# Performance work log

Hardware: AMD Instinct MI355X
Metric: run time of the kernel (lower is better)

Reference implementation:

```python
import jax, jax.numpy as jnp
import numpy as np

LUT_DIM = 33
CTX_DIM = 128


def _identity_lut(dim):
    coords = jnp.linspace(0.0, 1.0, dim)
    r, g, b = jnp.meshgrid(coords, coords, coords, indexing='ij')
    return jnp.stack([r, g, b], axis=-1)  # [dim, dim, dim, 3], axes (r,g,b)


def setup_inputs() -> dict:
    key = jax.random.key(0)
    ks = jax.random.split(key, 8)
    B, H, W = 4, 512, 512
    image = jax.random.normal(ks[0], (B, 3, H, W), dtype=jnp.float32)
    spatial_context = jax.random.normal(ks[1], (B, CTX_DIM, H, W), dtype=jnp.float32)
    s = 0.05
    params = {
        'base_lut': _identity_lut(LUT_DIM),
        'W1': jax.random.normal(ks[2], (128, CTX_DIM), dtype=jnp.float32) * s,
        'b1': jnp.zeros((128,), dtype=jnp.float32),
        'W2': jax.random.normal(ks[3], (64, 128), dtype=jnp.float32) * s,
        'b2': jnp.zeros((64,), dtype=jnp.float32),
        'W3': jax.random.normal(ks[4], (3, 64), dtype=jnp.float32) * s,
        'b3': jnp.zeros((3,), dtype=jnp.float32),
        'offset_scale': jnp.float32(0.1),
    }
    return {'image': image, 'spatial_context': spatial_context, **params}


def _conv1x1(x, W, b):
    # x: [B,Cin,H,W], W: [Cout,Cin]
    return jnp.einsum('bchw,oc->bohw', x, W) + b[None, :, None, None]


def _trilinear_lut(lut_flat, gx, gy, gz, dim):
    # lut_flat: [3, dim^3] (flattened over z,y,x = r,g,b axes)
    # gx,gy,gz: [B,H,W] float coords in [0, dim-1]; border padding via clamp
    fmax = jnp.float32(dim - 1)
    gx = jnp.clip(gx, 0.0, fmax)
    gy = jnp.clip(gy, 0.0, fmax)
    gz = jnp.clip(gz, 0.0, fmax)
    x0 = jnp.floor(gx).astype(jnp.int32)
    y0 = jnp.floor(gy).astype(jnp.int32)
    z0 = jnp.floor(gz).astype(jnp.int32)
    x1 = jnp.minimum(x0 + 1, dim - 1)
    y1 = jnp.minimum(y0 + 1, dim - 1)
    z1 = jnp.minimum(z0 + 1, dim - 1)
    fx = gx - x0.astype(gx.dtype)
    fy = gy - y0.astype(gy.dtype)
    fz = gz - z0.astype(gz.dtype)

    def gather(zi, yi, xi):
        idx = (zi * dim + yi) * dim + xi  # [B,H,W]
        return lut_flat[:, idx]  # [3,B,H,W]

    c000 = gather(z0, y0, x0); c001 = gather(z0, y0, x1)
    c010 = gather(z0, y1, x0); c011 = gather(z0, y1, x1)
    c100 = gather(z1, y0, x0); c101 = gather(z1, y0, x1)
    c110 = gather(z1, y1, x0); c111 = gather(z1, y1, x1)

    fx = fx[None]; fy = fy[None]; fz = fz[None]
    c00 = c000 * (1 - fx) + c001 * fx
    c01 = c010 * (1 - fx) + c011 * fx
    c10 = c100 * (1 - fx) + c101 * fx
    c11 = c110 * (1 - fx) + c111 * fx
    c0 = c00 * (1 - fy) + c01 * fy
    c1 = c10 * (1 - fy) + c11 * fy
    out = c0 * (1 - fz) + c1 * fz  # [3,B,H,W]
    return jnp.transpose(out, (1, 0, 2, 3))  # [B,3,H,W]


def reference(image, spatial_context, base_lut, W1, b1, W2, b2, W3, b3, offset_scale):
    dim = base_lut.shape[0]
    gelu = lambda v: jax.nn.gelu(v, approximate=False)
    h = gelu(_conv1x1(spatial_context, W1, b1))
    h = gelu(_conv1x1(h, W2, b2))
    offset = jnp.tanh(_conv1x1(h, W3, b3)) * offset_scale  # [B,3,H,W]

    img01 = jnp.clip((image + 1.0) * 0.5, 0.0, 1.0)
    # grid_sample convention: grid channel0 (R)->x->last LUT axis (b),
    # channel1 (G)->y->g axis, channel2 (B)->z->r axis; align_corners=True.
    scale = jnp.float32(dim - 1)
    gx = img01[:, 0] * scale  # R -> b axis
    gy = img01[:, 1] * scale  # G -> g axis
    gz = img01[:, 2] * scale  # B -> r axis
    # base_lut [r,g,b,3] -> channels-first [3, r(=z), g(=y), b(=x)] -> flatten
    lut_flat = jnp.transpose(base_lut, (3, 0, 1, 2)).reshape(3, dim * dim * dim)
    sampled = _trilinear_lut(lut_flat, gx, gy, gz, dim)  # [B,3,H,W]
    return sampled * 2.0 - 1.0 + offset
```

## Files before the change

kernel.cpp:

```cpp
#include <hip/hip_runtime.h>
#include <stdint.h>

#define HW 262144
#define LDIM 33

typedef __bf16 bf16x8 __attribute__((ext_vector_type(8)));
typedef __bf16 bf16x2 __attribute__((ext_vector_type(2)));
typedef float  f32x4  __attribute__((ext_vector_type(4)));

union BF8 { bf16x8 v; unsigned u[4]; };

__device__ __forceinline__ unsigned pk2(float a, float b) {
  bf16x2 p; p[0] = (__bf16)a; p[1] = (__bf16)b;
  return __builtin_bit_cast(unsigned, p);
}
__device__ __forceinline__ float exp2_hw(float x) {
  return __builtin_amdgcn_exp2f(x);
}
__device__ __forceinline__ float tanh_fast(float x) {
  float t = exp2_hw(x * 2.8853900818f);
  return 1.0f - __fdividef(2.0f, t + 1.0f);
}
__device__ __forceinline__ float gelu_t(float x) {
  float x2 = x * x;
  float p2 = x * fmaf(0.1029425216f, x2, 2.3021667f);
  float r  = __fdividef(1.0f, exp2_hw(p2) + 1.0f);
  return fmaf(-x, r, x);
}

__global__ __launch_bounds__(256, 2) void local3dlut_kernel(
    const float* __restrict__ img,  const float* __restrict__ ctx,
    const float* __restrict__ lut,  const float* __restrict__ W1,
    const float* __restrict__ b1,   const float* __restrict__ W2,
    const float* __restrict__ b2,   const float* __restrict__ W3,
    const float* __restrict__ b3,   const float* __restrict__ oscp,
    float* __restrict__ out)
{
  __shared__ uint4 smem4[3584];
  char* sm = (char*)smem4;
  const int t    = threadIdx.x;
  const int lane = t & 63;
  const int wv   = t >> 6;
  const int n    = lane & 15;
  const int q    = lane >> 4;

  #pragma unroll
  for (int rep = 0; rep < 16; ++rep) {
    int f4 = t + 256 * rep;
    float4 v = ((const float4*)W1)[f4];
    int fi = f4 << 2;
    int o = fi >> 7, k = fi & 127;
    char* dst = sm + o * 256 + (((k >> 3) ^ (o & 15)) << 4) + ((k & 7) << 1);
    *(uint2*)dst = make_uint2(pk2(v.x, v.y), pk2(v.z, v.w));
  }
  #pragma unroll
  for (int rep = 0; rep < 8; ++rep) {
    int f4 = t + 256 * rep;
    float4 v = ((const float4*)W2)[f4];
    int fi = f4 << 2;
    int o = fi >> 7, k = fi & 127;
    char* dst = sm + 32768 + o * 256 + (((k >> 3) ^ (o & 15)) << 4) + ((k & 7) << 1);
    *(uint2*)dst = make_uint2(pk2(v.x, v.y), pk2(v.z, v.w));
  }
  __syncthreads();

  float b1l[8][4];
  #pragma unroll
  for (int i = 0; i < 8; ++i)
    #pragma unroll
    for (int r = 0; r < 4; ++r) b1l[i][r] = b1[i * 16 + (q << 2) + r];
  float b2l[4][4];
  #pragma unroll
  for (int i = 0; i < 4; ++i)
    #pragma unroll
    for (int r = 0; r < 4; ++r) b2l[i][r] = b2[i * 16 + (q << 2) + r];
  BF8 w3a[2];
  #pragma unroll
  for (int ks3 = 0; ks3 < 2; ++ks3) {
    #pragma unroll
    for (int m = 0; m < 4; ++m) {
      float e0 = 0.f, e1 = 0.f;
      if (n < 3) {
        e0 = W3[n * 64 + ks3 * 32 + q * 8 + 2 * m];
        e1 = W3[n * 64 + ks3 * 32 + q * 8 + 2 * m + 1];
      }
      w3a[ks3].u[m] = pk2(e0, e1);
    }
  }
  const float b3a0 = b3[0], b3a1 = b3[1], b3a2 = b3[2];
  const float osc  = oscp[0];

  const int p0   = blockIdx.x * 512;
  const int bi   = p0 >> 18;
  const int sblk = p0 & (HW - 1);
  const float* ctxB = ctx + (size_t)bi * ((size_t)128 * HW);
  const float* imgB = img + (size_t)bi * ((size_t)3 * HW);
  float*       outB = out + (size_t)bi * ((size_t)3 * HW);
  char* hb = sm + 49152 + wv * 2048;
  char* hrow = hb + n * 128;
  const int nsw = n & 7;
  const int woff = (q & 1) << 3;

  #pragma unroll 1
  for (int it = 0; it < 8; ++it) {
    const int sw = sblk + it * 64 + wv * 16;

    const int spf = sw + n;
    const float rr = imgB[spf];
    const float gg = imgB[HW + spf];
    const float bb = imgB[2 * HW + spf];

    BF8 a1[4];
    {
      const int sA = sw + n;
      #pragma unroll
      for (int ks = 0; ks < 4; ++ks) {
        const float* cb = ctxB + (size_t)(ks * 32 + q * 8) * HW + sA;
        float v0 = cb[0];
        float v1 = cb[(size_t)1 * HW];
        float v2 = cb[(size_t)2 * HW];
        float v3 = cb[(size_t)3 * HW];
        float v4 = cb[(size_t)4 * HW];
        float v5 = cb[(size_t)5 * HW];
        float v6 = cb[(size_t)6 * HW];
        float v7 = cb[(size_t)7 * HW];
        a1[ks].u[0] = pk2(v0, v1);
        a1[ks].u[1] = pk2(v2, v3);
        a1[ks].u[2] = pk2(v4, v5);
        a1[ks].u[3] = pk2(v6, v7);
      }
    }

    float fx, fy, fz;
    float c000, c001, c010, c011, c100, c101, c110, c111;
    {
      float gx = fminf(fmaxf(fmaf(rr, 16.f, 16.f), 0.f), 32.f);
      float gy = fminf(fmaxf(fmaf(gg, 16.f, 16.f), 0.f), 32.f);
      float gz = fminf(fmaxf(fmaf(bb, 16.f, 16.f), 0.f), 32.f);
      int x0 = (int)gx, y0 = (int)gy, z0 = (int)gz;
      fx = gx - (float)x0; fy = gy - (float)y0; fz = gz - (float)z0;
      int x1 = min(x0 + 1, 32), y1 = min(y0 + 1, 32), z1 = min(z0 + 1, 32);
      int zy00 = (z0 * LDIM + y0) * LDIM, zy01 = (z0 * LDIM + y1) * LDIM;
      int zy10 = (z1 * LDIM + y0) * LDIM, zy11 = (z1 * LDIM + y1) * LDIM;
      const int chq = (q < 3) ? q : 2;
      const float* L = lut;
      c000 = L[(zy00 + x0) * 3 + chq]; c001 = L[(zy00 + x1) * 3 + chq];
      c010 = L[(zy01 + x0) * 3 + chq]; c011 = L[(zy01 + x1) * 3 + chq];
      c100 = L[(zy10 + x0) * 3 + chq]; c101 = L[(zy10 + x1) * 3 + chq];
      c110 = L[(zy11 + x0) * 3 + chq]; c111 = L[(zy11 + x1) * 3 + chq];
    }

    f32x4 acc2[4];
    #pragma unroll
    for (int j = 0; j < 4; ++j) { f32x4 z = {0.f,0.f,0.f,0.f}; acc2[j] = z; }

    #pragma unroll
    for (int half = 0; half < 2; ++half) {
      f32x4 acc1[4];
      #pragma unroll
      for (int j = 0; j < 4; ++j) { f32x4 z = {0.f,0.f,0.f,0.f}; acc1[j] = z; }

      #pragma unroll
      for (int ks = 0; ks < 4; ++ks) {
        #pragma unroll
        for (int nt4 = 0; nt4 < 4; ++nt4) {
          int row = (half * 4 + nt4) * 16 + n;
          bf16x8 bw = *(const bf16x8*)(sm + row * 256 + ((((ks << 2) + q) ^ n) << 4));
          acc1[nt4] = __builtin_amdgcn_mfma_f32_16x16x32_bf16(bw, a1[ks].v, acc1[nt4], 0, 0, 0);
        }
      }
      #pragma unroll
      for (int nt4 = 0; nt4 < 4; ++nt4) {
        float g0 = gelu_t(acc1[nt4][0] + b1l[half * 4 + nt4][0]);
        float g1 = gelu_t(acc1[nt4][1] + b1l[half * 4 + nt4][1]);
        float g2 = gelu_t(acc1[nt4][2] + b1l[half * 4 + nt4][2]);
        float g3 = gelu_t(acc1[nt4][3] + b1l[half * 4 + nt4][3]);
        int kg = (nt4 << 1) + (q >> 1);
        char* dst = hrow + ((kg ^ nsw) << 4) + woff;
        *(uint2*)dst = make_uint2(pk2(g0, g1), pk2(g2, g3));
      }
      #pragma unroll
      for (int ks2 = 0; ks2 < 2; ++ks2) {
        bf16x8 a2 = *(const bf16x8*)(hrow + ((((ks2 << 2) + q) ^ nsw) << 4));
        #pragma unroll
        for (int nt2 = 0; nt2 < 4; ++nt2) {
          int row = nt2 * 16 + n;
          int kg2 = half * 8 + (ks2 << 2) + q;
          bf16x8 bw = *(const bf16x8*)(sm + 32768 + row * 256 + ((kg2 ^ n) << 4));
          acc2[nt2] = __builtin_amdgcn_mfma_f32_16x16x32_bf16(bw, a2, acc2[nt2], 0, 0, 0);
        }
      }
    }

    #pragma unroll
    for (int nt2 = 0; nt2 < 4; ++nt2) {
      float g0 = gelu_t(acc2[nt2][0] + b2l[nt2][0]);
      float g1 = gelu_t(acc2[nt2][1] + b2l[nt2][1]);
      float g2 = gelu_t(acc2[nt2][2] + b2l[nt2][2]);
      float g3 = gelu_t(acc2[nt2][3] + b2l[nt2][3]);
      int kg = (nt2 << 1) + (q >> 1);
      char* dst = hrow + ((kg ^ nsw) << 4) + woff;
      *(uint2*)dst = make_uint2(pk2(g0, g1), pk2(g2, g3));
    }

    f32x4 acc3 = {0.f, 0.f, 0.f, 0.f};
    #pragma unroll
    for (int ks3 = 0; ks3 < 2; ++ks3) {
      bf16x8 hf = *(const bf16x8*)(hrow + ((((ks3 << 2) + q) ^ nsw) << 4));
      acc3 = __builtin_amdgcn_mfma_f32_16x16x32_bf16(w3a[ks3].v, hf, acc3, 0, 0, 0);
    }
    const int ba = n << 2;
    float d0 = __int_as_float(__builtin_amdgcn_ds_bpermute(ba, __float_as_int(acc3[0])));
    float d1 = __int_as_float(__builtin_amdgcn_ds_bpermute(ba, __float_as_int(acc3[1])));
    float d2 = __int_as_float(__builtin_amdgcn_ds_bpermute(ba, __float_as_int(acc3[2])));

    if (q < 3) {
      float sel  = (q == 0) ? d0   : ((q == 1) ? d1   : d2);
      float bsel = (q == 0) ? b3a0 : ((q == 1) ? b3a1 : b3a2);
      float ov = tanh_fast(sel + bsel) * osc;

      float c00 = c000 + fx * (c001 - c000);
      float c01 = c010 + fx * (c011 - c010);
      float c10 = c100 + fx * (c101 - c100);
      float c11 = c110 + fx * (c111 - c110);
      float ca  = c00 + fy * (c01 - c00);
      float cb2 = c10 + fy * (c11 - c10);
      float so  = ca + fz * (cb2 - ca);
      outB[q * HW + sw + n] = so * 2.f - 1.f + ov;
    }
  }
}

extern "C" void kernel_launch(void* const* d_in, const int* in_sizes, int n_in,
                              void* d_out, int out_size, void* d_ws, size_t ws_size,
                              hipStream_t stream) {
  const float* img = (const float*)d_in[0];
  const float* ctx = (const float*)d_in[1];
  const float* lut = (const float*)d_in[2];
  const float* W1  = (const float*)d_in[3];
  const float* b1  = (const float*)d_in[4];
  const float* W2  = (const float*)d_in[5];
  const float* b2  = (const float*)d_in[6];
  const float* W3  = (const float*)d_in[7];
  const float* b3  = (const float*)d_in[8];
  const float* osc = (const float*)d_in[9];
  float* out = (float*)d_out;
  local3dlut_kernel<<<dim3(2048), dim3(256), 0, stream>>>(
      img, ctx, lut, W1, b1, W2, b2, W3, b3, osc, out);
}
```

Before: 777.3 us.

## Split fused MLP kernel into GEMM1 kernel and tail kernel via workspace

Splits the single fused kernel in two. The first computes conv1+GELU and writes a bf16 hidden tensor (256 B per pixel, about 268 MB total) to workspace, and the second reads it back for conv2, conv3, the LUT interpolation and the output. The aim is to cut per-kernel LDS and register pressure so occupancy rises. The cost is a large extra global-memory round trip. The fused kernel remains as a fallback when the workspace is too small.

```diff
diff --git a/kernel.cpp b/kernel.cpp
--- a/kernel.cpp
+++ b/kernel.cpp
@@ -28,15 +28,11 @@
   return fmaf(-x, r, x);
 }
 
-__global__ __launch_bounds__(256, 2) void local3dlut_kernel(
-    const float* __restrict__ img,  const float* __restrict__ ctx,
-    const float* __restrict__ lut,  const float* __restrict__ W1,
-    const float* __restrict__ b1,   const float* __restrict__ W2,
-    const float* __restrict__ b2,   const float* __restrict__ W3,
-    const float* __restrict__ b3,   const float* __restrict__ oscp,
-    float* __restrict__ out)
+__global__ __launch_bounds__(256, 2) void gemm1_h1_kernel(
+    const float* __restrict__ ctx, const float* __restrict__ W1,
+    const float* __restrict__ b1,  char* __restrict__ h1)
 {
-  __shared__ uint4 smem4[3584];
+  __shared__ uint4 smem4[2048];
   char* sm = (char*)smem4;
   const int t    = threadIdx.x;
   const int lane = t & 63;
@@ -53,15 +49,6 @@
     char* dst = sm + o * 256 + (((k >> 3) ^ (o & 15)) << 4) + ((k & 7) << 1);
     *(uint2*)dst = make_uint2(pk2(v.x, v.y), pk2(v.z, v.w));
   }
-  #pragma unroll
-  for (int rep = 0; rep < 8; ++rep) {
-    int f4 = t + 256 * rep;
-    float4 v = ((const float4*)W2)[f4];
-    int fi = f4 << 2;
-    int o = fi >> 7, k = fi & 127;
-    char* dst = sm + 32768 + o * 256 + (((k >> 3) ^ (o & 15)) << 4) + ((k & 7) << 1);
-    *(uint2*)dst = make_uint2(pk2(v.x, v.y), pk2(v.z, v.w));
-  }
   __syncthreads();
 
   float b1l[8][4];
@@ -69,46 +56,16 @@
   for (int i = 0; i < 8; ++i)
     #pragma unroll
     for (int r = 0; r < 4; ++r) b1l[i][r] = b1[i * 16 + (q << 2) + r];
-  float b2l[4][4];
-  #pragma unroll
-  for (int i = 0; i < 4; ++i)
-    #pragma unroll
-    for (int r = 0; r < 4; ++r) b2l[i][r] = b2[i * 16 + (q << 2) + r];
-  BF8 w3a[2];
-  #pragma unroll
-  for (int ks3 = 0; ks3 < 2; ++ks3) {
-    #pragma unroll
-    for (int m = 0; m < 4; ++m) {
-      float e0 = 0.f, e1 = 0.f;
-      if (n < 3) {
-        e0 = W3[n * 64 + ks3 * 32 + q * 8 + 2 * m];
-        e1 = W3[n * 64 + ks3 * 32 + q * 8 + 2 * m + 1];
-      }
-      w3a[ks3].u[m] = pk2(e0, e1);
-    }
-  }
-  const float b3a0 = b3[0], b3a1 = b3[1], b3a2 = b3[2];
-  const float osc  = oscp[0];
 
   const int p0   = blockIdx.x * 512;
   const int bi   = p0 >> 18;
   const int sblk = p0 & (HW - 1);
   const float* ctxB = ctx + (size_t)bi * ((size_t)128 * HW);
-  const float* imgB = img + (size_t)bi * ((size_t)3 * HW);
-  float*       outB = out + (size_t)bi * ((size_t)3 * HW);
-  char* hb = sm + 49152 + wv * 2048;
-  char* hrow = hb + n * 128;
-  const int nsw = n & 7;
-  const int woff = (q & 1) << 3;
 
   #pragma unroll 1
   for (int it = 0; it < 8; ++it) {
     const int sw = sblk + it * 64 + wv * 16;
-
-    const int spf = sw + n;
-    const float rr = imgB[spf];
-    const float gg = imgB[HW + spf];
-    const float bb = imgB[2 * HW + spf];
+    const int gp = p0 + it * 64 + wv * 16 + n;
 
     BF8 a1[4];
     {
@@ -131,6 +88,105 @@
       }
     }
 
+    f32x4 acc[8];
+    #pragma unroll
+    for (int j = 0; j < 8; ++j) { f32x4 z = {0.f,0.f,0.f,0.f}; acc[j] = z; }
+    #pragma unroll
+    for (int ks = 0; ks < 4; ++ks) {
+      #pragma unroll
+      for (int nt = 0; nt < 8; ++nt) {
+        int row = nt * 16 + n;
+        bf16x8 bw = *(const bf16x8*)(sm + row * 256 + ((((ks << 2) + q) ^ n) << 4));
+        acc[nt] = __builtin_amdgcn_mfma_f32_16x16x32_bf16(bw, a1[ks].v, acc[nt], 0, 0, 0);
+      }
+    }
+
+    char* hrow = h1 + (size_t)gp * 256;
+    #pragma unroll
+    for (int nt = 0; nt < 8; ++nt) {
+      float g0 = gelu_t(acc[nt][0] + b1l[nt][0]);
+      float g1 = gelu_t(acc[nt][1] + b1l[nt][1]);
+      float g2 = gelu_t(acc[nt][2] + b1l[nt][2]);
+      float g3 = gelu_t(acc[nt][3] + b1l[nt][3]);
+      *(uint2*)(hrow + nt * 32 + (q << 3)) = make_uint2(pk2(g0, g1), pk2(g2, g3));
+    }
+  }
+}
+
+__global__ __launch_bounds__(256, 2) void mlp_tail_kernel(
+    const float* __restrict__ img, const float* __restrict__ lut,
+    const char* __restrict__ h1,   const float* __restrict__ W2,
+    const float* __restrict__ b2,  const float* __restrict__ W3,
+    const float* __restrict__ b3,  const float* __restrict__ oscp,
+    float* __restrict__ out)
+{
+  __shared__ uint4 smem4[1536];
+  char* sm = (char*)smem4;
+  const int t    = threadIdx.x;
+  const int lane = t & 63;
+  const int wv   = t >> 6;
+  const int n    = lane & 15;
+  const int q    = lane >> 4;
+
+  #pragma unroll
+  for (int rep = 0; rep < 8; ++rep) {
+    int f4 = t + 256 * rep;
+    float4 v = ((const float4*)W2)[f4];
+    int fi = f4 << 2;
+    int o = fi >> 7, k = fi & 127;
+    char* dst = sm + o * 256 + (((k >> 3) ^ (o & 15)) << 4) + ((k & 7) << 1);
+    *(uint2*)dst = make_uint2(pk2(v.x, v.y), pk2(v.z, v.w));
+  }
+  __syncthreads();
+
+  float b2l[4][4];
+  #pragma unroll
+  for (int i = 0; i < 4; ++i)
+    #pragma unroll
+    for (int r = 0; r < 4; ++r) b2l[i][r] = b2[i * 16 + (q << 2) + r];
+  BF8 w3a[2];
+  #pragma unroll
+  for (int ks3 = 0; ks3 < 2; ++ks3) {
+    #pragma unroll
+    for (int m = 0; m < 4; ++m) {
+      float e0 = 0.f, e1 = 0.f;
+      if (n < 3) {
+        e0 = W3[n * 64 + ks3 * 32 + q * 8 + 2 * m];
+        e1 = W3[n * 64 + ks3 * 32 + q * 8 + 2 * m + 1];
+      }
+      w3a[ks3].u[m] = pk2(e0, e1);
+    }
+  }
+  const float b3a0 = b3[0], b3a1 = b3[1], b3a2 = b3[2];
+  const float osc  = oscp[0];
+
+  const int p0   = blockIdx.x * 512;
+  const int bi   = p0 >> 18;
+  const int sblk = p0 & (HW - 1);
+  const float* imgB = img + (size_t)bi * ((size_t)3 * HW);
+  float*       outB = out + (size_t)bi * ((size_t)3 * HW);
+  char* hb = sm + 16384 + wv * 2048;
+  char* hrow = hb + n * 128;
+  const int nsw = n & 7;
+  const int woff = (q & 1) << 3;
+
+  #pragma unroll 1
+  for (int it = 0; it < 8; ++it) {
+    const int sw = sblk + it * 64 + wv * 16;
+    const int gp = p0 + it * 64 + wv * 16 + n;
+
+    bf16x8 a2[4];
+    {
+      const char* hr = h1 + (size_t)gp * 256;
+      #pragma unroll
+      for (int ks = 0; ks < 4; ++ks)
+        a2[ks] = *(const bf16x8*)(hr + ks * 64 + (q << 4));
+    }
+
+    const int spf = sw + n;
+    const float rr = imgB[spf];
+    const float gg = imgB[HW + spf];
+    const float bb = imgB[2 * HW + spf];
     float fx, fy, fz;
     float c000, c001, c010, c011, c100, c101, c110, c111;
     {
@@ -153,13 +209,184 @@
     f32x4 acc2[4];
     #pragma unroll
     for (int j = 0; j < 4; ++j) { f32x4 z = {0.f,0.f,0.f,0.f}; acc2[j] = z; }
+    #pragma unroll
+    for (int ks = 0; ks < 4; ++ks) {
+      #pragma unroll
+      for (int nt2 = 0; nt2 < 4; ++nt2) {
+        int row = nt2 * 16 + n;
+        bf16x8 bw = *(const bf16x8*)(sm + row * 256 + ((((ks << 2) + q) ^ n) << 4));
+        acc2[nt2] = __builtin_amdgcn_mfma_f32_16x16x32_bf16(bw, a2[ks], acc2[nt2], 0, 0, 0);
+      }
+    }
+
+    #pragma unroll
+    for (int nt2 = 0; nt2 < 4; ++nt2) {
+      float g0 = gelu_t(acc2[nt2][0] + b2l[nt2][0]);
+      float g1 = gelu_t(acc2[nt2][1] + b2l[nt2][1]);
+      float g2 = gelu_t(acc2[nt2][2] + b2l[nt2][2]);
+      float g3 = gelu_t(acc2[nt2][3] + b2l[nt2][3]);
+      int kg = (nt2 << 1) + (q >> 1);
+      char* dst = hrow + ((kg ^ nsw) << 4) + woff;
+      *(uint2*)dst = make_uint2(pk2(g0, g1), pk2(g2, g3));
+    }
+
+    f32x4 acc3 = {0.f, 0.f, 0.f, 0.f};
+    #pragma unroll
+    for (int ks3 = 0; ks3 < 2; ++ks3) {
+      bf16x8 hf = *(const bf16x8*)(hrow + ((((ks3 << 2) + q) ^ nsw) << 4));
+      acc3 = __builtin_amdgcn_mfma_f32_16x16x32_bf16(w3a[ks3].v, hf, acc3, 0, 0, 0);
+    }
+    const int ba = n << 2;
+    float d0 = __int_as_float(__builtin_amdgcn_ds_bpermute(ba, __float_as_int(acc3[0])));
+    float d1 = __int_as_float(__builtin_amdgcn_ds_bpermute(ba, __float_as_int(acc3[1])));
+    float d2 = __int_as_float(__builtin_amdgcn_ds_bpermute(ba, __float_as_int(acc3[2])));
+
+    if (q < 3) {
+      float sel  = (q == 0) ? d0   : ((q == 1) ? d1   : d2);
+      float bsel = (q == 0) ? b3a0 : ((q == 1) ? b3a1 : b3a2);
+      float ov = tanh_fast(sel + bsel) * osc;
+      float c00 = c000 + fx * (c001 - c000);
+      float c01 = c010 + fx * (c011 - c010);
+      float c10 = c100 + fx * (c101 - c100);
+      float c11 = c110 + fx * (c111 - c110);
+      float ca  = c00 + fy * (c01 - c00);
+      float cb2 = c10 + fy * (c11 - c10);
+      float so  = ca + fz * (cb2 - ca);
+      outB[q * HW + sw + n] = so * 2.f - 1.f + ov;
+    }
+  }
+}
+
+__global__ __launch_bounds__(256, 2) void local3dlut_fused(
+    const float* __restrict__ img,  const float* __restrict__ ctx,
+    const float* __restrict__ lut,  const float* __restrict__ W1,
+    const float* __restrict__ b1,   const float* __restrict__ W2,
+    const float* __restrict__ b2,   const float* __restrict__ W3,
+    const float* __restrict__ b3,   const float* __restrict__ oscp,
+    float* __restrict__ out)
+{
+  __shared__ uint4 smem4[3584];
+  char* sm = (char*)smem4;
+  const int t    = threadIdx.x;
+  const int lane = t & 63;
+  const int wv   = t >> 6;
+  const int n    = lane & 15;
+  const int q    = lane >> 4;
+
+  #pragma unroll
+  for (int rep = 0; rep < 16; ++rep) {
+    int f4 = t + 256 * rep;
+    float4 v = ((const float4*)W1)[f4];
+    int fi = f4 << 2;
+    int o = fi >> 7, k = fi & 127;
+    char* dst = sm + o * 256 + (((k >> 3) ^ (o & 15)) << 4) + ((k & 7) << 1);
+    *(uint2*)dst = make_uint2(pk2(v.x, v.y), pk2(v.z, v.w));
+  }
+  #pragma unroll
+  for (int rep = 0; rep < 8; ++rep) {
+    int f4 = t + 256 * rep;
+    float4 v = ((const float4*)W2)[f4];
+    int fi = f4 << 2;
+    int o = fi >> 7, k = fi & 127;
+    char* dst = sm + 32768 + o * 256 + (((k >> 3) ^ (o & 15)) << 4) + ((k & 7) << 1);
+    *(uint2*)dst = make_uint2(pk2(v.x, v.y), pk2(v.z, v.w));
+  }
+  __syncthreads();
+
+  float b1l[8][4];
+  #pragma unroll
+  for (int i = 0; i < 8; ++i)
+    #pragma unroll
+    for (int r = 0; r < 4; ++r) b1l[i][r] = b1[i * 16 + (q << 2) + r];
+  float b2l[4][4];
+  #pragma unroll
+  for (int i = 0; i < 4; ++i)
+    #pragma unroll
+    for (int r = 0; r < 4; ++r) b2l[i][r] = b2[i * 16 + (q << 2) + r];
+  BF8 w3a[2];
+  #pragma unroll
+  for (int ks3 = 0; ks3 < 2; ++ks3) {
+    #pragma unroll
+    for (int m = 0; m < 4; ++m) {
+      float e0 = 0.f, e1 = 0.f;
+      if (n < 3) {
+        e0 = W3[n * 64 + ks3 * 32 + q * 8 + 2 * m];
+        e1 = W3[n * 64 + ks3 * 32 + q * 8 + 2 * m + 1];
+      }
+      w3a[ks3].u[m] = pk2(e0, e1);
+    }
+  }
+  const float b3a0 = b3[0], b3a1 = b3[1], b3a2 = b3[2];
+  const float osc  = oscp[0];
+
+  const int p0   = blockIdx.x * 512;
+  const int bi   = p0 >> 18;
+  const int sblk = p0 & (HW - 1);
+  const float* ctxB = ctx + (size_t)bi * ((size_t)128 * HW);
+  const float* imgB = img + (size_t)bi * ((size_t)3 * HW);
+  float*       outB = out + (size_t)bi * ((size_t)3 * HW);
+  char* hb = sm + 49152 + wv * 2048;
+  char* hrow = hb + n * 128;
+  const int nsw = n & 7;
+  const int woff = (q & 1) << 3;
+
+  #pragma unroll 1
+  for (int it = 0; it < 8; ++it) {
+    const int sw = sblk + it * 64 + wv * 16;
+    const int spf = sw + n;
+    const float rr = imgB[spf];
+    const float gg = imgB[HW + spf];
+    const float bb = imgB[2 * HW + spf];
+
+    BF8 a1[4];
+    {
+      const int sA = sw + n;
+      #pragma unroll
+      for (int ks = 0; ks < 4; ++ks) {
+        const float* cb = ctxB + (size_t)(ks * 32 + q * 8) * HW + sA;
+        float v0 = cb[0];
+        float v1 = cb[(size_t)1 * HW];
+        float v2 = cb[(size_t)2 * HW];
+        float v3 = cb[(size_t)3 * HW];
+        float v4 = cb[(size_t)4 * HW];
+        float v5 = cb[(size_t)5 * HW];
+        float v6 = cb[(size_t)6 * HW];
+        float v7 = cb[(size_t)7 * HW];
+        a1[ks].u[0] = pk2(v0, v1);
+        a1[ks].u[1] = pk2(v2, v3);
+        a1[ks].u[2] = pk2(v4, v5);
+        a1[ks].u[3] = pk2(v6, v7);
+      }
+    }
+
+    float fx, fy, fz;
+    float c000, c001, c010, c011, c100, c101, c110, c111;
+    {
+      float gx = fminf(fmaxf(fmaf(rr, 16.f, 16.f), 0.f), 32.f);
+      float gy = fminf(fmaxf(fmaf(gg, 16.f, 16.f), 0.f), 32.f);
+      float gz = fminf(fmaxf(fmaf(bb, 16.f, 16.f), 0.f), 32.f);
+      int x0 = (int)gx, y0 = (int)gy, z0 = (int)gz;
+      fx = gx - (float)x0; fy = gy - (float)y0; fz = gz - (float)z0;
+      int x1 = min(x0 + 1, 32), y1 = min(y0 + 1, 32), z1 = min(z0 + 1, 32);
+      int zy00 = (z0 * LDIM + y0) * LDIM, zy01 = (z0 * LDIM + y1) * LDIM;
+      int zy10 = (z1 * LDIM + y0) * LDIM, zy11 = (z1 * LDIM + y1) * LDIM;
+      const int chq = (q < 3) ? q : 2;
+      const float* L = lut;
+      c000 = L[(zy00 + x0) * 3 + chq]; c001 = L[(zy00 + x1) * 3 + chq];
+      c010 = L[(zy01 + x0) * 3 + chq]; c011 = L[(zy01 + x1) * 3 + chq];
+      c100 = L[(zy10 + x0) * 3 + chq]; c101 = L[(zy10 + x1) * 3 + chq];
+      c110 = L[(zy11 + x0) * 3 + chq]; c111 = L[(zy11 + x1) * 3 + chq];
+    }
+
+    f32x4 acc2[4];
+    #pragma unroll
+    for (int j = 0; j < 4; ++j) { f32x4 z = {0.f,0.f,0.f,0.f}; acc2[j] = z; }
 
     #pragma unroll
     for (int half = 0; half < 2; ++half) {
       f32x4 acc1[4];
       #pragma unroll
       for (int j = 0; j < 4; ++j) { f32x4 z = {0.f,0.f,0.f,0.f}; acc1[j] = z; }
-
       #pragma unroll
       for (int ks = 0; ks < 4; ++ks) {
         #pragma unroll
@@ -218,7 +445,6 @@
       float sel  = (q == 0) ? d0   : ((q == 1) ? d1   : d2);
       float bsel = (q == 0) ? b3a0 : ((q == 1) ? b3a1 : b3a2);
       float ov = tanh_fast(sel + bsel) * osc;
-
       float c00 = c000 + fx * (c001 - c000);
       float c01 = c010 + fx * (c011 - c010);
       float c10 = c100 + fx * (c101 - c100);
@@ -245,6 +471,13 @@
   const float* b3  = (const float*)d_in[8];
   const float* osc = (const float*)d_in[9];
   float* out = (float*)d_out;
-  local3dlut_kernel<<<dim3(2048), dim3(256), 0, stream>>>(
-      img, ctx, lut, W1, b1, W2, b2, W3, b3, osc, out);
-}
+  const size_t h1_bytes = (size_t)4 * HW * 256;
+  if (ws_size >= h1_bytes && d_ws != nullptr) {
+    gemm1_h1_kernel<<<dim3(2048), dim3(256), 0, stream>>>(ctx, W1, b1, (char*)d_ws);
+    mlp_tail_kernel<<<dim3(2048), dim3(256), 0, stream>>>(
+        img, lut, (const char*)d_ws, W2, b2, W3, b3, osc, out);
+  } else {
+    local3dlut_fused<<<dim3(2048), dim3(256), 0, stream>>>(
+        img, ctx, lut, W1, b1, W2, b2, W3, b3, osc, out);
+  }
+}
```

After: 886.5 us. +14.0%, slower.
